# Optimization experiments

Measured on AMD Instinct MI355X. Metric: run time of the kernel, lower is better.

The kernel has to match this reference:

```python
import jax, jax.numpy as jnp
import numpy as np

N, E, F_IN, E_DIM, H, G = 8192, 40960, 32, 8, 64, 64
EPS = 1e-5


def _lin(key, fan_in, fan_out):
    k1, k2 = jax.random.split(key)
    s = 1.0 / np.sqrt(fan_in)
    w = jax.random.uniform(k1, (fan_in, fan_out), jnp.float32, -s, s)
    b = jax.random.uniform(k2, (fan_out,), jnp.float32, -s, s)
    return w, b


def setup_inputs() -> dict:
    key = jax.random.key(0)
    ks = jax.random.split(key, 32)
    inp = {}
    inp['x'] = jax.random.normal(ks[0], (N, F_IN), jnp.float32)
    inp['edge_index'] = jax.random.randint(ks[1], (2, E), 0, N)
    inp['edge_attr'] = jax.random.normal(ks[2], (E, E_DIM), jnp.float32)
    inp['batch'] = jnp.sort(jax.random.randint(ks[3], (N,), 0, G))
    # NNConv 1 (F_IN -> H)
    inp['e1_w1'], inp['e1_b1'] = _lin(ks[4], E_DIM, H)
    inp['e1_w2'], inp['e1_b2'] = _lin(ks[5], H, F_IN * H)
    inp['root1_w'], inp['root1_b'] = _lin(ks[6], F_IN, H)
    inp['bn1_g'] = jnp.ones((H,), jnp.float32); inp['bn1_b'] = jnp.zeros((H,), jnp.float32)
    # NNConv 2 (H -> H)
    inp['e2_w1'], inp['e2_b1'] = _lin(ks[7], E_DIM, H)
    inp['e2_w2'], inp['e2_b2'] = _lin(ks[8], H, H * H)
    inp['root2_w'], inp['root2_b'] = _lin(ks[9], H, H)
    inp['bn2_g'] = jnp.ones((H,), jnp.float32); inp['bn2_b'] = jnp.zeros((H,), jnp.float32)
    # NNConv 3 (H -> H)
    inp['e3_w1'], inp['e3_b1'] = _lin(ks[10], E_DIM, H)
    inp['e3_w2'], inp['e3_b2'] = _lin(ks[11], H, H * H)
    inp['root3_w'], inp['root3_b'] = _lin(ks[12], H, H)
    inp['bn3_g'] = jnp.ones((H,), jnp.float32); inp['bn3_b'] = jnp.zeros((H,), jnp.float32)
    # attention gate MLP: H -> H//2 -> 1
    inp['gate_w1'], inp['gate_b1'] = _lin(ks[13], H, H // 2)
    inp['gate_w2'], inp['gate_b2'] = _lin(ks[14], H // 2, 1)
    # fc head: H -> 2H (BN, relu) -> H (BN, relu) -> 1
    inp['fc1_w'], inp['fc1_b'] = _lin(ks[15], H, 2 * H)
    inp['fcbn1_g'] = jnp.ones((2 * H,), jnp.float32); inp['fcbn1_b'] = jnp.zeros((2 * H,), jnp.float32)
    inp['fc2_w'], inp['fc2_b'] = _lin(ks[16], 2 * H, H)
    inp['fcbn2_g'] = jnp.ones((H,), jnp.float32); inp['fcbn2_b'] = jnp.zeros((H,), jnp.float32)
    inp['fc3_w'], inp['fc3_b'] = _lin(ks[17], H, 1)
    return inp


def _bn(x, g, b):
    # training-mode batch norm over node/graph dim
    m = jnp.mean(x, axis=0)
    v = jnp.var(x, axis=0)
    return (x - m) * jax.lax.rsqrt(v + EPS) * g + b


def _nnconv(x, edge_index, edge_attr, w1, b1, w2, b2, root_w, root_b, in_ch, out_ch):
    src, dst = edge_index[0], edge_index[1]
    h = jax.nn.relu(edge_attr @ w1 + b1)                     # [E, H]
    We = (h @ w2 + b2).reshape(-1, in_ch, out_ch)            # [E, in, out]
    msg = jnp.einsum('ei,eio->eo', x[src], We)               # [E, out]
    s = jax.ops.segment_sum(msg, dst, num_segments=N)
    cnt = jax.ops.segment_sum(jnp.ones((msg.shape[0],), x.dtype), dst, num_segments=N)
    agg = s / jnp.clip(cnt, 1.0)[:, None]                    # mean aggregation
    return agg + x @ root_w + root_b


def _global_attention(x, batch, gw1, gb1, gw2, gb2):
    gate = jax.nn.relu(x @ gw1 + gb1) @ gw2 + gb2            # [N, 1]
    gate = gate[:, 0]
    m = jax.ops.segment_max(gate, batch, num_segments=G)
    e = jnp.exp(gate - m[batch])
    z = jax.ops.segment_sum(e, batch, num_segments=G)
    alpha = e / z[batch]
    return jax.ops.segment_sum(alpha[:, None] * x, batch, num_segments=G)  # [G, H]


def reference(x, edge_index, edge_attr, batch,
              e1_w1, e1_b1, e1_w2, e1_b2, root1_w, root1_b, bn1_g, bn1_b,
              e2_w1, e2_b1, e2_w2, e2_b2, root2_w, root2_b, bn2_g, bn2_b,
              e3_w1, e3_b1, e3_w2, e3_b2, root3_w, root3_b, bn3_g, bn3_b,
              gate_w1, gate_b1, gate_w2, gate_b2,
              fc1_w, fc1_b, fcbn1_g, fcbn1_b, fc2_w, fc2_b, fcbn2_g, fcbn2_b, fc3_w, fc3_b):
    x1 = jax.nn.relu(_bn(_nnconv(x, edge_index, edge_attr, e1_w1, e1_b1, e1_w2, e1_b2, root1_w, root1_b, F_IN, H), bn1_g, bn1_b))
    x2 = jax.nn.relu(_bn(_nnconv(x1, edge_index, edge_attr, e2_w1, e2_b1, e2_w2, e2_b2, root2_w, root2_b, H, H), bn2_g, bn2_b)) + x1
    x3 = jax.nn.relu(_bn(_nnconv(x2, edge_index, edge_attr, e3_w1, e3_b1, e3_w2, e3_b2, root3_w, root3_b, H, H), bn3_g, bn3_b)) + x2
    # dropout is identity in eval/reference mode
    p = _global_attention(x3, batch, gate_w1, gate_b1, gate_w2, gate_b2)  # [G, H]
    h = jax.nn.relu(_bn(p @ fc1_w + fc1_b, fcbn1_g, fcbn1_b))
    h = jax.nn.relu(_bn(h @ fc2_w + fc2_b, fcbn2_g, fcbn2_b))
    out = h @ fc3_w + fc3_b
    return out[:, 0]
```

## Files before the change

kernel.cpp:

```cpp
#include <hip/hip_runtime.h>
#include <hip/hip_bf16.h>

#define NN 8192
#define EE 40960
#define FIN 32
#define HH 64
#define GG 64

typedef __attribute__((ext_vector_type(4))) float f32x4;
typedef __attribute__((ext_vector_type(8))) short s16x8;
typedef unsigned short ushort_t;

__device__ __forceinline__ unsigned short f2bf(float f) {
    union { float f; unsigned int u; } v; v.f = f;
    unsigned int u = v.u;
    return (unsigned short)((u + 0x7fffu + ((u >> 16) & 1u)) >> 16);
}

__device__ __forceinline__ void gll16(const void* g, void* l) {
    __builtin_amdgcn_global_load_lds((__attribute__((address_space(1))) void*)g,
                                     (__attribute__((address_space(3))) void*)l, 16, 0, 0);
}

__global__ void btbuild_all_kernel(const float* __restrict__ w2a, const float* __restrict__ b2a, ushort_t* __restrict__ Bta,
                                   const float* __restrict__ w2b, const float* __restrict__ b2b, ushort_t* __restrict__ Btb,
                                   const float* __restrict__ w2c, const float* __restrict__ b2c, ushort_t* __restrict__ Btc,
                                   int* __restrict__ cnt, int* __restrict__ fill, float* __restrict__ stats) {
    int bid = blockIdx.x;
    int t = threadIdx.x;
    if (bid < 32) { cnt[bid * 256 + t] = 0; fill[bid * 256 + t] = 0; }
    if (bid == 32) stats[t] = 0.f;
    if (bid == 33 && t < 128) stats[256 + t] = 0.f;

    const float* w2; const float* b2; ushort_t* Bt; int IC; int base;
    if (bid < 520)       { w2 = w2a; b2 = b2a; Bt = Bta; IC = 32; base = bid; }
    else if (bid < 1560) { w2 = w2b; b2 = b2b; Bt = Btb; IC = 64; base = bid - 520; }
    else                 { w2 = w2c; b2 = b2c; Bt = Btc; IC = 64; base = bid - 1560; }
    int CH = IC >> 3;
    int flat = base * 256 + t;
    if (flat >= 64 * 65 * IC) return;
    int s = flat / (64 * IC);
    int rem = flat - s * (64 * IC);
    int row = rem / IC;
    int j = rem - row * IC;
    int q = j >> 3, w = j & 7;
    int c = q ^ (row & (CH - 1));
    int i = c * 8 + w;
    float v = (s < 64) ? w2[s * (IC * 64) + i * 64 + row] : b2[i * 64 + row];
    Bt[flat] = f2bf(v);
}

__global__ void hist_kernel(const int* __restrict__ dst, int* __restrict__ cnt) {
    int e = blockIdx.x * 256 + threadIdx.x;
    if (e < EE) atomicAdd(&cnt[dst[e]], 1);
}

__global__ void scan_kernel(const int* __restrict__ cnt, int* __restrict__ row_ptr) {
    __shared__ int lds[1024];
    int t = threadIdx.x;
    int v[8]; int s = 0;
    int base = t * 8;
#pragma unroll
    for (int j = 0; j < 8; j++) { v[j] = s; s += cnt[base + j]; }
    lds[t] = s;
    __syncthreads();
    for (int off = 1; off < 1024; off <<= 1) {
        int add = (t >= off) ? lds[t - off] : 0;
        __syncthreads();
        lds[t] += add;
        __syncthreads();
    }
    int ex = lds[t] - s;
#pragma unroll
    for (int j = 0; j < 8; j++) row_ptr[base + j] = ex + v[j];
    if (t == 1023) row_ptr[NN] = lds[1023];
}

__global__ void scatter_kernel(const int* __restrict__ dst, const int* __restrict__ row_ptr,
                               int* __restrict__ fill, int* __restrict__ perm) {
    int e = blockIdx.x * 256 + threadIdx.x;
    if (e < EE) {
        int d = dst[e];
        int pos = row_ptr[d] + atomicAdd(&fill[d], 1);
        perm[pos] = e;
    }
}

template<int IC>
__launch_bounds__(256, 4)
__global__ void conv_msg_kernel(const float* __restrict__ eattr,
                                const float* __restrict__ w1,
                                const float* __restrict__ b1,
                                const float* __restrict__ xin,
                                const int* __restrict__ src,
                                const int* __restrict__ perm,
                                const ushort_t* __restrict__ Bt,
                                float* __restrict__ msg) {
    constexpr int NKK  = IC / 32;
    constexpr int CH   = IC / 8;
    constexpr int TILE = IC * 64;
    constexpr int NQ   = (TILE * 2) / 4096;
    __shared__ ushort_t bt_lds[2][TILE];
    __shared__ float h_t[4096];
    __shared__ float ea_s[64][9];
    __shared__ float w1s[512];
    __shared__ float b1s[64];
    __shared__ int eid_s[64];

    const int t = threadIdx.x;
    const int wave = t >> 6;
    const int l = t & 63;
    const int g = l >> 4;
    const int rlo = l & 15;
    const int e0 = blockIdx.x * 64;

    if (t < 64) { eid_s[t] = perm[e0 + t]; b1s[t] = b1[t]; }
    for (int i = t; i < 512; i += 256) w1s[i] = w1[i];
    __syncthreads();

    auto stage = [&](int buf, int step) {
#pragma unroll
        for (int q = 0; q < NQ; ++q) {
            int off = q * 2048 + wave * 512;
            const ushort_t* gp = Bt + (size_t)step * TILE + off + l * 8;
            gll16(gp, &bt_lds[buf][off]);
        }
    };

    stage(0, 0);

#pragma unroll
    for (int j = 0; j < 2; j++) {
        int idx = t + 256 * j;
        int e = idx >> 3, i = idx & 7;
        ea_s[e][i] = eattr[(size_t)eid_s[e] * 8 + i];
    }

    s16x8 afrag[4][NKK];
#pragma unroll
    for (int m = 0; m < 4; ++m) {
        int row = m * 16 + rlo;
        int sn = src[eid_s[row]];
        const float* xp = xin + (size_t)sn * IC + g * 8;
#pragma unroll
        for (int kk = 0; kk < NKK; ++kk) {
            f32x4 a = *(const f32x4*)(xp + kk * 32);
            f32x4 b = *(const f32x4*)(xp + kk * 32 + 4);
            s16x8 fr;
            fr[0] = (short)f2bf(a[0]); fr[1] = (short)f2bf(a[1]);
            fr[2] = (short)f2bf(a[2]); fr[3] = (short)f2bf(a[3]);
            fr[4] = (short)f2bf(b[0]); fr[5] = (short)f2bf(b[1]);
            fr[6] = (short)f2bf(b[2]); fr[7] = (short)f2bf(b[3]);
            afrag[m][kk] = fr;
        }
    }
    __syncthreads();

#pragma unroll
    for (int j = 0; j < 16; ++j) {
        int k = wave * 16 + j;
        float s = b1s[k];
#pragma unroll
        for (int i = 0; i < 8; i++) s += ea_s[l][i] * w1s[i * 64 + k];
        h_t[(k << 6) + l] = fmaxf(s, 0.f);
    }
    __syncthreads();

    f32x4 acc[4];
#pragma unroll
    for (int m = 0; m < 4; m++) acc[m] = (f32x4){0.f, 0.f, 0.f, 0.f};

    const int bcol = wave * 16 + rlo;
    const int bmask = bcol & (CH - 1);
    const f32x4 zf = (f32x4){0.f, 0.f, 0.f, 0.f};

    for (int step = 0; step < 65; ++step) {
        if (step < 64) stage((step + 1) & 1, step + 1);
        const int buf = step & 1;
        s16x8 bfr[NKK];
#pragma unroll
        for (int kk = 0; kk < NKK; kk++) {
            int q = (kk * 4 + g) ^ bmask;
            bfr[kk] = *(const s16x8*)&bt_lds[buf][bcol * IC + q * 8];
        }
#pragma unroll
        for (int m = 0; m < 4; m++) {
            f32x4 P = __builtin_amdgcn_mfma_f32_16x16x32_bf16(afrag[m][0], bfr[0], zf, 0, 0, 0);
            if constexpr (NKK == 2)
                P = __builtin_amdgcn_mfma_f32_16x16x32_bf16(afrag[m][1], bfr[1], P, 0, 0, 0);
            if (step == 64) {
                acc[m] += P;
            } else {
                f32x4 h4 = *(const f32x4*)&h_t[(step << 6) + m * 16 + (g << 2)];
                acc[m] += h4 * P;
            }
        }
        __syncthreads();
    }

#pragma unroll
    for (int m = 0; m < 4; m++) {
        int row = e0 + m * 16 + (g << 2);
        float* mp = msg + (size_t)row * 64 + wave * 16 + rlo;
        mp[0] = acc[m][0]; mp[64] = acc[m][1]; mp[128] = acc[m][2]; mp[192] = acc[m][3];
    }
}

__global__ void aggregate_kernel(const float* __restrict__ msg, const int* __restrict__ row_ptr,
                                 const float* __restrict__ xin, int IC,
                                 const float* __restrict__ root_w, const float* __restrict__ root_b,
                                 float* __restrict__ y, float* __restrict__ stats) {
    int t = threadIdx.x;
    int n = blockIdx.x * 16 + (t >> 4);
    int cg = (t & 15) * 4;
    int s = row_ptr[n], e = row_ptr[n + 1];
    f32x4 acc = (f32x4){0.f, 0.f, 0.f, 0.f};
    for (int j = s; j < e; ++j) {
        acc += *(const f32x4*)&msg[(size_t)j * 64 + cg];
    }
    float inv = 1.0f / fmaxf((float)(e - s), 1.0f);
    acc *= inv;
    const float* xr = xin + (size_t)n * IC;
    for (int i = 0; i < IC; ++i) {
        float xv = xr[i];
        acc += xv * (*(const f32x4*)&root_w[i * 64 + cg]);
    }
    acc += *(const f32x4*)&root_b[cg];
    *(f32x4*)&y[(size_t)n * 64 + cg] = acc;

    f32x4 a2 = acc * acc;
#pragma unroll
    for (int j = 0; j < 4; j++) {
        acc[j] += __shfl_xor(acc[j], 16); acc[j] += __shfl_xor(acc[j], 32);
        a2[j]  += __shfl_xor(a2[j], 16);  a2[j]  += __shfl_xor(a2[j], 32);
    }
    __shared__ float ls[4][64], lq[4][64];
    int w = t >> 6;
    if ((t & 63) < 16) {
#pragma unroll
        for (int j = 0; j < 4; j++) { ls[w][cg + j] = acc[j]; lq[w][cg + j] = a2[j]; }
    }
    __syncthreads();
    if (t < 64) {
        float S = ls[0][t] + ls[1][t] + ls[2][t] + ls[3][t];
        float Q = lq[0][t] + lq[1][t] + lq[2][t] + lq[3][t];
        atomicAdd(&stats[t], S);
        atomicAdd(&stats[64 + t], Q);
    }
}

__global__ void bn_apply_kernel(const float* __restrict__ y, const float* __restrict__ stats,
                                const float* __restrict__ gam, const float* __restrict__ bet,
                                const float* __restrict__ res, float* __restrict__ xout) {
    int i4 = blockIdx.x * 256 + threadIdx.x;
    int cg = (i4 & 15) * 4;
    const float invN = 1.0f / (float)NN;
    f32x4 yv = *(const f32x4*)&y[(size_t)i4 * 4];
    f32x4 o;
#pragma unroll
    for (int j = 0; j < 4; j++) {
        int c = cg + j;
        float mean = stats[c] * invN;
        float var = stats[64 + c] * invN - mean * mean;
        float sc = rsqrtf(var + 1e-5f) * gam[c];
        float v = (yv[j] - mean) * sc + bet[c];
        o[j] = fmaxf(v, 0.f);
    }
    if (res) o += *(const f32x4*)&res[(size_t)i4 * 4];
    *(f32x4*)&xout[(size_t)i4 * 4] = o;
}

__global__ void bn_gate_kernel(const float* __restrict__ y, const float* __restrict__ stats,
                               const float* __restrict__ gam, const float* __restrict__ bet,
                               const float* __restrict__ res, float* __restrict__ xout,
                               const float* __restrict__ gw1, const float* __restrict__ gb1,
                               const float* __restrict__ gw2, const float* __restrict__ gb2,
                               float* __restrict__ gate) {
    __shared__ float x3s[64][68];
    __shared__ float w1s[2048];
    __shared__ float b1s[32], w2s[32];
    __shared__ float b2s;
    int t = threadIdx.x;
    for (int i = t; i < 2048; i += 256) w1s[i] = gw1[i];
    if (t < 32) { b1s[t] = gb1[t]; w2s[t] = gw2[t]; }
    if (t == 0) b2s = gb2[0];
    const float invN = 1.0f / (float)NN;
    size_t base4 = (size_t)blockIdx.x * 1024;
#pragma unroll
    for (int j = 0; j < 4; j++) {
        int i4l = j * 256 + t;
        int row = i4l >> 4, cg = (i4l & 15) * 4;
        f32x4 yv = *(const f32x4*)&y[(base4 + i4l) * 4];
        f32x4 o;
#pragma unroll
        for (int jj = 0; jj < 4; jj++) {
            int c = cg + jj;
            float mean = stats[c] * invN;
            float var = stats[64 + c] * invN - mean * mean;
            float sc = rsqrtf(var + 1e-5f) * gam[c];
            o[jj] = fmaxf((yv[jj] - mean) * sc + bet[c], 0.f);
        }
        o += *(const f32x4*)&res[(base4 + i4l) * 4];
        *(f32x4*)&xout[(base4 + i4l) * 4] = o;
        *(f32x4*)&x3s[row][cg] = o;
    }
    __syncthreads();
    int w = t >> 6, l = t & 63;
    int row = w * 16 + (l >> 2), part = l & 3;
    float hacc[8];
#pragma unroll
    for (int j = 0; j < 8; j++) hacc[j] = b1s[part * 8 + j];
    for (int i = 0; i < 64; i++) {
        float xv = x3s[row][i];
#pragma unroll
        for (int j = 0; j < 8; j++) hacc[j] += xv * w1s[i * 32 + part * 8 + j];
    }
    float gv = 0.f;
#pragma unroll
    for (int j = 0; j < 8; j++) gv += fmaxf(hacc[j], 0.f) * w2s[part * 8 + j];
    gv += __shfl_xor(gv, 1); gv += __shfl_xor(gv, 2);
    if (part == 0) gate[blockIdx.x * 64 + row] = gv + b2s;
}

__global__ void attn_pool_kernel(const float* __restrict__ x3, const float* __restrict__ gate,
                                 const int* __restrict__ batch, float* __restrict__ p) {
    int g = blockIdx.x;
    int t = threadIdx.x;
    int lo = 0, hi = NN;
    while (lo < hi) { int mid = (lo + hi) >> 1; if (batch[mid] < g) lo = mid + 1; else hi = mid; }
    int s = lo;
    hi = NN;
    while (lo < hi) { int mid = (lo + hi) >> 1; if (batch[mid] < g + 1) lo = mid + 1; else hi = mid; }
    int e = lo;

    __shared__ float red[4];
    __shared__ float sM, sZ;
    float m = -1e30f;
    for (int n = s + t; n < e; n += 256) m = fmaxf(m, gate[n]);
#pragma unroll
    for (int off = 1; off < 64; off <<= 1) m = fmaxf(m, __shfl_xor(m, off));
    if ((t & 63) == 0) red[t >> 6] = m;
    __syncthreads();
    if (t == 0) sM = fmaxf(fmaxf(red[0], red[1]), fmaxf(red[2], red[3]));
    __syncthreads();
    float z = 0.f;
    for (int n = s + t; n < e; n += 256) z += __expf(gate[n] - sM);
#pragma unroll
    for (int off = 1; off < 64; off <<= 1) z += __shfl_xor(z, off);
    if ((t & 63) == 0) red[t >> 6] = z;
    __syncthreads();
    if (t == 0) sZ = red[0] + red[1] + red[2] + red[3];
    __syncthreads();
    int w = t >> 6, c = t & 63;
    float acc = 0.f;
    for (int n = s + w; n < e; n += 4) acc += __expf(gate[n] - sM) * x3[(size_t)n * 64 + c];
    __shared__ float pa[4][64];
    pa[w][c] = acc;
    __syncthreads();
    if (t < 64) {
        float v = pa[0][t] + pa[1][t] + pa[2][t] + pa[3][t];
        p[g * 64 + t] = (sZ > 0.f) ? v / sZ : 0.f;
    }
}

__global__ void head1_kernel(const float* __restrict__ p, const float* __restrict__ fc1w,
                             const float* __restrict__ fc1b, const float* __restrict__ bn1g,
                             const float* __restrict__ bn1b, float* __restrict__ t1n) {
    __shared__ float sp[64 * 65];
    __shared__ float w1s[64 * 16];
    __shared__ float t1s[64 * 17];
    __shared__ float sA[16], sB[16];
    int t = threadIdx.x;
    int c0 = blockIdx.x * 16;
    for (int i = t; i < 4096; i += 256) { int r = i >> 6, cc = i & 63; sp[r * 65 + cc] = p[i]; }
    for (int i = t; i < 1024; i += 256) { int r = i >> 4, cc = i & 15; w1s[i] = fc1w[r * 128 + c0 + cc]; }
    __syncthreads();
    int r16 = t >> 4, c = t & 15;
    float b = fc1b[c0 + c];
#pragma unroll
    for (int rb = 0; rb < 4; rb++) {
        int row = rb * 16 + r16;
        float s = b;
#pragma unroll 8
        for (int i = 0; i < 64; i++) s += sp[row * 65 + i] * w1s[i * 16 + c];
        t1s[row * 17 + c] = s;
    }
    __syncthreads();
    if (t < 16) {
        float su = 0.f, sq = 0.f;
        for (int r = 0; r < 64; r++) { float v = t1s[r * 17 + t]; su += v; sq += v * v; }
        float mean = su * (1.f / 64.f), var = sq * (1.f / 64.f) - mean * mean;
        float sc = rsqrtf(var + 1e-5f) * bn1g[c0 + t];
        sA[t] = sc; sB[t] = bn1b[c0 + t] - mean * sc;
    }
    __syncthreads();
#pragma unroll
    for (int rb = 0; rb < 4; rb++) {
        int row = rb * 16 + r16;
        float v = t1s[row * 17 + c] * sA[c] + sB[c];
        t1n[row * 128 + c0 + c] = fmaxf(v, 0.f);
    }
}

__global__ void head2_kernel(const float* __restrict__ t1n, const float* __restrict__ fc2w,
                             const float* __restrict__ fc2b, const float* __restrict__ bn2g,
                             const float* __restrict__ bn2b, float* __restrict__ y2n) {
    __shared__ float t1sh[64 * 129];
    __shared__ float w2s[128 * 8];
    __shared__ float t2s[64 * 9];
    __shared__ float sA[8], sB[8];
    int t = threadIdx.x;
    int c0 = blockIdx.x * 8;
    for (int i = t; i < 8192; i += 256) { int r = i >> 7, cc = i & 127; t1sh[r * 129 + cc] = t1n[i]; }
    for (int i = t; i < 1024; i += 256) { int r = i >> 3, cc = i & 7; w2s[i] = fc2w[r * 64 + c0 + cc]; }
    __syncthreads();
    int r32 = t >> 3, c = t & 7;
    float b = fc2b[c0 + c];
#pragma unroll
    for (int rb = 0; rb < 2; rb++) {
        int row = rb * 32 + r32;
        float s = b;
#pragma unroll 8
        for (int i = 0; i < 128; i++) s += t1sh[row * 129 + i] * w2s[i * 8 + c];
        t2s[row * 9 + c] = s;
    }
    __syncthreads();
    if (t < 8) {
        float su = 0.f, sq = 0.f;
        for (int r = 0; r < 64; r++) { float v = t2s[r * 9 + t]; su += v; sq += v * v; }
        float mean = su * (1.f / 64.f), var = sq * (1.f / 64.f) - mean * mean;
        float sc = rsqrtf(var + 1e-5f) * bn2g[c0 + t];
        sA[t] = sc; sB[t] = bn2b[c0 + t] - mean * sc;
    }
    __syncthreads();
#pragma unroll
    for (int rb = 0; rb < 2; rb++) {
        int row = rb * 32 + r32;
        float v = t2s[row * 9 + c] * sA[c] + sB[c];
        y2n[row * 64 + c0 + c] = fmaxf(v, 0.f);
    }
}

__global__ void head3_kernel(const float* __restrict__ y2n, const float* __restrict__ fc3w,
                             const float* __restrict__ fc3b, float* __restrict__ out) {
    __shared__ float w3[64];
    int t = threadIdx.x;
    w3[t] = fc3w[t];
    __syncthreads();
    float s = fc3b[0];
    const float* yr = y2n + t * 64;
#pragma unroll 8
    for (int i = 0; i < 64; i++) s += yr[i] * w3[i];
    out[t] = s;
}

extern "C" void kernel_launch(void* const* d_in, const int* in_sizes, int n_in,
                              void* d_out, int out_size, void* d_ws, size_t ws_size,
                              hipStream_t stream) {
    const float* x     = (const float*)d_in[0];
    const int*   eidx  = (const int*)d_in[1];
    const float* eattr = (const float*)d_in[2];
    const int*   batch = (const int*)d_in[3];
    const float* e1w1 = (const float*)d_in[4];  const float* e1b1 = (const float*)d_in[5];
    const float* e1w2 = (const float*)d_in[6];  const float* e1b2 = (const float*)d_in[7];
    const float* r1w  = (const float*)d_in[8];  const float* r1b  = (const float*)d_in[9];
    const float* bn1g = (const float*)d_in[10]; const float* bn1b = (const float*)d_in[11];
    const float* e2w1 = (const float*)d_in[12]; const float* e2b1 = (const float*)d_in[13];
    const float* e2w2 = (const float*)d_in[14]; const float* e2b2 = (const float*)d_in[15];
    const float* r2w  = (const float*)d_in[16]; const float* r2b  = (const float*)d_in[17];
    const float* bn2g = (const float*)d_in[18]; const float* bn2b = (const float*)d_in[19];
    const float* e3w1 = (const float*)d_in[20]; const float* e3b1 = (const float*)d_in[21];
    const float* e3w2 = (const float*)d_in[22]; const float* e3b2 = (const float*)d_in[23];
    const float* r3w  = (const float*)d_in[24]; const float* r3b  = (const float*)d_in[25];
    const float* bn3g = (const float*)d_in[26]; const float* bn3b = (const float*)d_in[27];
    const float* gw1  = (const float*)d_in[28]; const float* gb1  = (const float*)d_in[29];
    const float* gw2  = (const float*)d_in[30]; const float* gb2  = (const float*)d_in[31];
    const float* fc1w = (const float*)d_in[32]; const float* fc1b = (const float*)d_in[33];
    const float* fbn1g= (const float*)d_in[34]; const float* fbn1b= (const float*)d_in[35];
    const float* fc2w = (const float*)d_in[36]; const float* fc2b = (const float*)d_in[37];
    const float* fbn2g= (const float*)d_in[38]; const float* fbn2b= (const float*)d_in[39];
    const float* fc3w = (const float*)d_in[40]; const float* fc3b = (const float*)d_in[41];
    float* out = (float*)d_out;

    const int* src = eidx;
    const int* dst = eidx + EE;

    char* ws = (char*)d_ws;
    size_t off = 0;
    auto take = [&](size_t n) { void* p = ws + off; off = (off + n + 255) & ~(size_t)255; return p; };
    ushort_t* Bt1 = (ushort_t*)take(64 * 2080 * 2 + 256);
    ushort_t* Bt2 = (ushort_t*)take(64 * 4160 * 2 + 256);
    ushort_t* Bt3 = (ushort_t*)take(64 * 4160 * 2 + 256);
    float* msg  = (float*)take((size_t)EE * 64 * 4);
    float* ybuf = (float*)take((size_t)NN * 64 * 4);
    float* x1   = (float*)take((size_t)NN * 64 * 4);
    float* x2   = (float*)take((size_t)NN * 64 * 4);
    float* x3   = (float*)take((size_t)NN * 64 * 4);
    float* gate = (float*)take((size_t)NN * 4);
    float* pbuf = (float*)take(64 * 64 * 4);
    float* t1n  = (float*)take(64 * 128 * 4);
    float* y2n  = (float*)take(64 * 64 * 4);
    float* stats = (float*)take(384 * 4);
    int* cnt  = (int*)take((size_t)NN * 4);
    int* fill = (int*)take((size_t)NN * 4);
    int* rowp = (int*)take((size_t)(NN + 1) * 4);
    int* perm = (int*)take((size_t)EE * 4);

    btbuild_all_kernel<<<2600, 256, 0, stream>>>(e1w2, e1b2, Bt1, e2w2, e2b2, Bt2,
                                                 e3w2, e3b2, Bt3, cnt, fill, stats);
    hist_kernel<<<160, 256, 0, stream>>>(dst, cnt);
    scan_kernel<<<1, 1024, 0, stream>>>(cnt, rowp);
    scatter_kernel<<<160, 256, 0, stream>>>(dst, rowp, fill, perm);

    conv_msg_kernel<32><<<640, 256, 0, stream>>>(eattr, e1w1, e1b1, x, src, perm, Bt1, msg);
    aggregate_kernel<<<512, 256, 0, stream>>>(msg, rowp, x, 32, r1w, r1b, ybuf, stats);
    bn_apply_kernel<<<512, 256, 0, stream>>>(ybuf, stats, bn1g, bn1b, nullptr, x1);

    conv_msg_kernel<64><<<640, 256, 0, stream>>>(eattr, e2w1, e2b1, x1, src, perm, Bt2, msg);
    aggregate_kernel<<<512, 256, 0, stream>>>(msg, rowp, x1, 64, r2w, r2b, ybuf, stats + 128);
    bn_apply_kernel<<<512, 256, 0, stream>>>(ybuf, stats + 128, bn2g, bn2b, x1, x2);

    conv_msg_kernel<64><<<640, 256, 0, stream>>>(eattr, e3w1, e3b1, x2, src, perm, Bt3, msg);
    aggregate_kernel<<<512, 256, 0, stream>>>(msg, rowp, x2, 64, r3w, r3b, ybuf, stats + 256);
    bn_gate_kernel<<<128, 256, 0, stream>>>(ybuf, stats + 256, bn3g, bn3b, x2, x3,
                                            gw1, gb1, gw2, gb2, gate);

    attn_pool_kernel<<<64, 256, 0, stream>>>(x3, gate, batch, pbuf);
    head1_kernel<<<8, 256, 0, stream>>>(pbuf, fc1w, fc1b, fbn1g, fbn1b, t1n);
    head2_kernel<<<8, 256, 0, stream>>>(t1n, fc2w, fc2b, fbn2g, fbn2b, y2n);
    head3_kernel<<<1, 64, 0, stream>>>(y2n, fc3w, fc3b, out);
}
```

Before: 281.4 us.

## Per-wave private B tiles with 4-deep async prefetch, removing block barriers

Each wave now stages only its own 16-column slice of the Bt tile into a private LDS region. A 4-buffer ring with three tiles in flight replaces the shared double buffer. Per-step __syncthreads is replaced by an s_waitcnt vmcnt wait on that wave's own global_load_lds ops, so waves stop stalling on each other and more load latency is hidden. The risks are extra LDS (a 4x4 buffer array), which may lower occupancy at 4 blocks per CU, and a reliance on vmcnt ordering and LDS visibility without an explicit barrier. Steps past 64 are clamped to reload the last tile so the wait counts stay uniform.

Measured after the change: 264.2 us. 6.1% less time.

```diff
diff --git a/kernel.cpp b/kernel.cpp
--- a/kernel.cpp
+++ b/kernel.cpp
@@ -99,8 +99,9 @@
     constexpr int NKK  = IC / 32;
     constexpr int CH   = IC / 8;
     constexpr int TILE = IC * 64;
-    constexpr int NQ   = (TILE * 2) / 4096;
-    __shared__ ushort_t bt_lds[2][TILE];
+    constexpr int WT   = IC * 16;
+    constexpr int NQ   = (WT * 2) / 1024;
+    __shared__ ushort_t bt_lds[4][4][WT];
     __shared__ float h_t[4096];
     __shared__ float ea_s[64][9];
     __shared__ float w1s[512];
@@ -117,17 +118,6 @@
     if (t < 64) { eid_s[t] = perm[e0 + t]; b1s[t] = b1[t]; }
     for (int i = t; i < 512; i += 256) w1s[i] = w1[i];
     __syncthreads();
-
-    auto stage = [&](int buf, int step) {
-#pragma unroll
-        for (int q = 0; q < NQ; ++q) {
-            int off = q * 2048 + wave * 512;
-            const ushort_t* gp = Bt + (size_t)step * TILE + off + l * 8;
-            gll16(gp, &bt_lds[buf][off]);
-        }
-    };
-
-    stage(0, 0);
 
 #pragma unroll
     for (int j = 0; j < 2; j++) {
@@ -166,22 +156,33 @@
     }
     __syncthreads();
 
+    auto stage = [&](int step) {
+        int s2 = step > 64 ? 64 : step;
+        ushort_t* lp = &bt_lds[step & 3][wave][0];
+        const ushort_t* gp = Bt + (size_t)s2 * TILE + wave * WT + l * 8;
+        gll16(gp, lp);
+        if constexpr (NQ == 2) gll16(gp + 512, lp + 512);
+    };
+
+    stage(0); stage(1); stage(2);
+
     f32x4 acc[4];
 #pragma unroll
     for (int m = 0; m < 4; m++) acc[m] = (f32x4){0.f, 0.f, 0.f, 0.f};
 
-    const int bcol = wave * 16 + rlo;
-    const int bmask = bcol & (CH - 1);
+    const int bmask = rlo & (CH - 1);
     const f32x4 zf = (f32x4){0.f, 0.f, 0.f, 0.f};
 
     for (int step = 0; step < 65; ++step) {
-        if (step < 64) stage((step + 1) & 1, step + 1);
-        const int buf = step & 1;
+        if constexpr (NQ == 2) asm volatile("s_waitcnt vmcnt(4)" ::: "memory");
+        else                   asm volatile("s_waitcnt vmcnt(2)" ::: "memory");
+        __builtin_amdgcn_sched_barrier(0);
+        const ushort_t* wbuf = &bt_lds[step & 3][wave][0];
         s16x8 bfr[NKK];
 #pragma unroll
         for (int kk = 0; kk < NKK; kk++) {
             int q = (kk * 4 + g) ^ bmask;
-            bfr[kk] = *(const s16x8*)&bt_lds[buf][bcol * IC + q * 8];
+            bfr[kk] = *(const s16x8*)&wbuf[rlo * IC + q * 8];
         }
 #pragma unroll
         for (int m = 0; m < 4; m++) {
@@ -195,7 +196,7 @@
                 acc[m] += h4 * P;
             }
         }
-        __syncthreads();
+        stage(step + 3);
     }
 
 #pragma unroll
```

## Process 128 edges per block in conv_msg to reuse staged weight tiles

Applied to the files above, without the earlier changes.

Each conv_msg block now handles two 64-edge groups, so every bf16 weight tile staged into LDS feeds twice as many MFMAs. The aim is to halve global weight traffic, LDS staging and barrier count per edge. In exchange the grid halves to 320 blocks, register pressure doubles (launch bounds lowered to 2 blocks per SM), and the h_t LDS buffer doubles in size. Workspace sizing for the Bt buffers is also rewritten.

Result: slower. 298.9 us (+6.2%).

```diff
diff --git a/kernel.cpp b/kernel.cpp
--- a/kernel.cpp
+++ b/kernel.cpp
@@ -87,7 +87,7 @@
 }
 
 template<int IC>
-__launch_bounds__(256, 4)
+__launch_bounds__(256, 2)
 __global__ void conv_msg_kernel(const float* __restrict__ eattr,
                                 const float* __restrict__ w1,
                                 const float* __restrict__ b1,
@@ -101,22 +101,18 @@
     constexpr int TILE = IC * 64;
     constexpr int NQ   = (TILE * 2) / 4096;
     __shared__ ushort_t bt_lds[2][TILE];
-    __shared__ float h_t[4096];
-    __shared__ float ea_s[64][9];
+    __shared__ float h_t[2][4096];
+    __shared__ float ea_s[128][9];
     __shared__ float w1s[512];
     __shared__ float b1s[64];
-    __shared__ int eid_s[64];
+    __shared__ int eid_s[128];
 
     const int t = threadIdx.x;
     const int wave = t >> 6;
     const int l = t & 63;
     const int g = l >> 4;
     const int rlo = l & 15;
-    const int e0 = blockIdx.x * 64;
-
-    if (t < 64) { eid_s[t] = perm[e0 + t]; b1s[t] = b1[t]; }
-    for (int i = t; i < 512; i += 256) w1s[i] = w1[i];
-    __syncthreads();
+    const int e0 = blockIdx.x * 128;
 
     auto stage = [&](int buf, int step) {
 #pragma unroll
@@ -129,29 +125,37 @@
 
     stage(0, 0);
 
-#pragma unroll
-    for (int j = 0; j < 2; j++) {
+    if (t < 128) eid_s[t] = perm[e0 + t];
+    if (t < 64) b1s[t] = b1[t];
+    for (int i = t; i < 512; i += 256) w1s[i] = w1[i];
+    __syncthreads();
+
+#pragma unroll
+    for (int j = 0; j < 4; j++) {
         int idx = t + 256 * j;
         int e = idx >> 3, i = idx & 7;
         ea_s[e][i] = eattr[(size_t)eid_s[e] * 8 + i];
     }
 
-    s16x8 afrag[4][NKK];
-#pragma unroll
-    for (int m = 0; m < 4; ++m) {
-        int row = m * 16 + rlo;
-        int sn = src[eid_s[row]];
-        const float* xp = xin + (size_t)sn * IC + g * 8;
-#pragma unroll
-        for (int kk = 0; kk < NKK; ++kk) {
-            f32x4 a = *(const f32x4*)(xp + kk * 32);
-            f32x4 b = *(const f32x4*)(xp + kk * 32 + 4);
-            s16x8 fr;
-            fr[0] = (short)f2bf(a[0]); fr[1] = (short)f2bf(a[1]);
-            fr[2] = (short)f2bf(a[2]); fr[3] = (short)f2bf(a[3]);
-            fr[4] = (short)f2bf(b[0]); fr[5] = (short)f2bf(b[1]);
-            fr[6] = (short)f2bf(b[2]); fr[7] = (short)f2bf(b[3]);
-            afrag[m][kk] = fr;
+    s16x8 afrag[2][4][NKK];
+#pragma unroll
+    for (int g2 = 0; g2 < 2; ++g2) {
+#pragma unroll
+        for (int m = 0; m < 4; ++m) {
+            int row = g2 * 64 + m * 16 + rlo;
+            int sn = src[eid_s[row]];
+            const float* xp = xin + (size_t)sn * IC + g * 8;
+#pragma unroll
+            for (int kk = 0; kk < NKK; ++kk) {
+                f32x4 a = *(const f32x4*)(xp + kk * 32);
+                f32x4 b = *(const f32x4*)(xp + kk * 32 + 4);
+                s16x8 fr;
+                fr[0] = (short)f2bf(a[0]); fr[1] = (short)f2bf(a[1]);
+                fr[2] = (short)f2bf(a[2]); fr[3] = (short)f2bf(a[3]);
+                fr[4] = (short)f2bf(b[0]); fr[5] = (short)f2bf(b[1]);
+                fr[6] = (short)f2bf(b[2]); fr[7] = (short)f2bf(b[3]);
+                afrag[g2][m][kk] = fr;
+            }
         }
     }
     __syncthreads();
@@ -159,16 +163,22 @@
 #pragma unroll
     for (int j = 0; j < 16; ++j) {
         int k = wave * 16 + j;
-        float s = b1s[k];
-#pragma unroll
-        for (int i = 0; i < 8; i++) s += ea_s[l][i] * w1s[i * 64 + k];
-        h_t[(k << 6) + l] = fmaxf(s, 0.f);
-    }
-    __syncthreads();
-
-    f32x4 acc[4];
-#pragma unroll
-    for (int m = 0; m < 4; m++) acc[m] = (f32x4){0.f, 0.f, 0.f, 0.f};
+#pragma unroll
+        for (int g2 = 0; g2 < 2; ++g2) {
+            int e = g2 * 64 + l;
+            float s = b1s[k];
+#pragma unroll
+            for (int i = 0; i < 8; i++) s += ea_s[e][i] * w1s[i * 64 + k];
+            h_t[g2][(k << 6) + l] = fmaxf(s, 0.f);
+        }
+    }
+    __syncthreads();
+
+    f32x4 acc[2][4];
+#pragma unroll
+    for (int g2 = 0; g2 < 2; g2++)
+#pragma unroll
+        for (int m = 0; m < 4; m++) acc[g2][m] = (f32x4){0.f, 0.f, 0.f, 0.f};
 
     const int bcol = wave * 16 + rlo;
     const int bmask = bcol & (CH - 1);
@@ -184,25 +194,32 @@
             bfr[kk] = *(const s16x8*)&bt_lds[buf][bcol * IC + q * 8];
         }
 #pragma unroll
+        for (int g2 = 0; g2 < 2; g2++) {
+#pragma unroll
+            for (int m = 0; m < 4; m++) {
+                f32x4 P = __builtin_amdgcn_mfma_f32_16x16x32_bf16(afrag[g2][m][0], bfr[0], zf, 0, 0, 0);
+                if constexpr (NKK == 2)
+                    P = __builtin_amdgcn_mfma_f32_16x16x32_bf16(afrag[g2][m][1], bfr[1], P, 0, 0, 0);
+                if (step == 64) {
+                    acc[g2][m] += P;
+                } else {
+                    f32x4 h4 = *(const f32x4*)&h_t[g2][(step << 6) + m * 16 + (g << 2)];
+                    acc[g2][m] += h4 * P;
+                }
+            }
+        }
+        __syncthreads();
+    }
+
+#pragma unroll
+    for (int g2 = 0; g2 < 2; g2++) {
+#pragma unroll
         for (int m = 0; m < 4; m++) {
-            f32x4 P = __builtin_amdgcn_mfma_f32_16x16x32_bf16(afrag[m][0], bfr[0], zf, 0, 0, 0);
-            if constexpr (NKK == 2)
-                P = __builtin_amdgcn_mfma_f32_16x16x32_bf16(afrag[m][1], bfr[1], P, 0, 0, 0);
-            if (step == 64) {
-                acc[m] += P;
-            } else {
-                f32x4 h4 = *(const f32x4*)&h_t[(step << 6) + m * 16 + (g << 2)];
-                acc[m] += h4 * P;
-            }
-        }
-        __syncthreads();
-    }
-
-#pragma unroll
-    for (int m = 0; m < 4; m++) {
-        int row = e0 + m * 16 + (g << 2);
-        float* mp = msg + (size_t)row * 64 + wave * 16 + rlo;
-        mp[0] = acc[m][0]; mp[64] = acc[m][1]; mp[128] = acc[m][2]; mp[192] = acc[m][3];
+            int row = e0 + g2 * 64 + m * 16 + (g << 2);
+            float* mp = msg + (size_t)row * 64 + wave * 16 + rlo;
+            mp[0] = acc[g2][m][0]; mp[64] = acc[g2][m][1];
+            mp[128] = acc[g2][m][2]; mp[192] = acc[g2][m][3];
+        }
     }
 }
 
@@ -488,9 +505,9 @@
     char* ws = (char*)d_ws;
     size_t off = 0;
     auto take = [&](size_t n) { void* p = ws + off; off = (off + n + 255) & ~(size_t)255; return p; };
-    ushort_t* Bt1 = (ushort_t*)take(64 * 2080 * 2 + 256);
-    ushort_t* Bt2 = (ushort_t*)take(64 * 4160 * 2 + 256);
-    ushort_t* Bt3 = (ushort_t*)take(64 * 4160 * 2 + 256);
+    ushort_t* Bt1 = (ushort_t*)take((size_t)65 * 2048 * 2);
+    ushort_t* Bt2 = (ushort_t*)take((size_t)65 * 4096 * 2);
+    ushort_t* Bt3 = (ushort_t*)take((size_t)65 * 4096 * 2);
     float* msg  = (float*)take((size_t)EE * 64 * 4);
     float* ybuf = (float*)take((size_t)NN * 64 * 4);
     float* x1   = (float*)take((size_t)NN * 64 * 4);
@@ -512,15 +529,15 @@
     scan_kernel<<<1, 1024, 0, stream>>>(cnt, rowp);
     scatter_kernel<<<160, 256, 0, stream>>>(dst, rowp, fill, perm);
 
-    conv_msg_kernel<32><<<640, 256, 0, stream>>>(eattr, e1w1, e1b1, x, src, perm, Bt1, msg);
+    conv_msg_kernel<32><<<320, 256, 0, stream>>>(eattr, e1w1, e1b1, x, src, perm, Bt1, msg);
     aggregate_kernel<<<512, 256, 0, stream>>>(msg, rowp, x, 32, r1w, r1b, ybuf, stats);
     bn_apply_kernel<<<512, 256, 0, stream>>>(ybuf, stats, bn1g, bn1b, nullptr, x1);
 
-    conv_msg_kernel<64><<<640, 256, 0, stream>>>(eattr, e2w1, e2b1, x1, src, perm, Bt2, msg);
+    conv_msg_kernel<64><<<320, 256, 0, stream>>>(eattr, e2w1, e2b1, x1, src, perm, Bt2, msg);
     aggregate_kernel<<<512, 256, 0, stream>>>(msg, rowp, x1, 64, r2w, r2b, ybuf, stats + 128);
     bn_apply_kernel<<<512, 256, 0, stream>>>(ybuf, stats + 128, bn2g, bn2b, x1, x2);
 
-    conv_msg_kernel<64><<<640, 256, 0, stream>>>(eattr, e3w1, e3b1, x2, src, perm, Bt3, msg);
+    conv_msg_kernel<64><<<320, 256, 0, stream>>>(eattr, e3w1, e3b1, x2, src, perm, Bt3, msg);
     aggregate_kernel<<<512, 256, 0, stream>>>(msg, rowp, x2, 64, r3w, r3b, ybuf, stats + 256);
     bn_gate_kernel<<<128, 256, 0, stream>>>(ybuf, stats + 256, bn3g, bn3b, x2, x3,
                                             gw1, gb1, gw2, gb2, gate);
```
